# Kernel tuning notes

Measured on AMD Instinct MI355X. Metric: run time of the kernel, lower is better.

The kernel has to match this reference:

```python
import jax, jax.numpy as jnp
import numpy as np

C = 128   # channel_num
S = 56    # spatial size
K = 3     # ksize -> gaussian kernel is 2K x 2K = 6x6


def _gaussian_bank(theta, p, sig, a):
    # Vectorized version of get_gaussian over all (i, u) channel pairs.
    coords = jnp.linspace(-K, K, 2 * K)
    xv, yv = jnp.meshgrid(coords, coords, indexing='ij')  # [2K, 2K]
    ct = jnp.cos(theta)[:, :, None, None]                  # [C, C, 1, 1]
    st = jnp.sin(theta)[:, :, None, None]
    xrot = xv * ct + yv * st                               # [C, C, 2K, 2K]
    yrot = -xv * st + yv * ct
    p2 = (p ** 2)[:, :, None, None]
    s2 = (sig ** 2)[:, :, None, None]
    amp = (a / (2.0 * jnp.pi * p * sig))[:, :, None, None]
    return amp * jnp.exp(-0.5 * (xrot ** 2 / p2 + yrot ** 2 / s2))  # [C, C, 2K, 2K]


def setup_inputs() -> dict:
    key = jax.random.key(0)
    ks = jax.random.split(key, 8)
    scale = 90.0
    theta = scale * jnp.abs(jax.random.normal(ks[0], (C, C)))
    p = scale * jnp.abs(jax.random.normal(ks[1], (C, C))) + 10.0
    sig = scale * jnp.abs(jax.random.normal(ks[2], (C, C))) + 10.0
    a = scale * jnp.abs(jax.random.normal(ks[3], (C, C)))
    nI = jnp.abs(jax.random.normal(ks[4], (C, C)))
    nU = jnp.abs(jax.random.normal(ks[5], (C,)))
    bias = jnp.abs(jax.random.normal(ks[6], (C,)))
    # positive activations (module assumes post-ReLU input; pow of negatives -> NaN)
    x = jax.random.uniform(ks[7], (2, C, S, S), dtype=jnp.float32)
    return {"x": x, "theta": theta, "p": p, "sig": sig, "a": a,
            "nI": nI, "nU": nU, "bias": bias}


def reference(x, theta, p, sig, a, nI, nU, bias):
    B = x.shape[0]
    g = _gaussian_bank(theta, p, sig, a)                     # [C, C, 2K, 2K]
    # x[b,i]^nI[i,u] for all pairs -> [B, C, C, S, S]
    xp = x[:, :, None, :, :] ** nI[None, :, :, None, None]
    xp = xp.reshape(B, C * C, S, S)
    kern = g.reshape(C * C, 1, 2 * K, 2 * K)
    # depthwise cross-correlation per (i,u) pair; even kernel + pad K -> S+1,
    # then crop first row/col (matches output[1:, 1:] in the torch code)
    conv = jax.lax.conv_general_dilated(
        xp, kern, window_strides=(1, 1), padding=((K, K), (K, K)),
        feature_group_count=C * C)                           # [B, C*C, S+1, S+1]
    conv = conv[:, :, 1:, 1:].reshape(B, C, C, S, S)
    denom = (bias ** nU)[None, :, None, None] + conv.sum(axis=2)  # [B, C, S, S]
    num = x ** nU[None, :, None, None]
    return num / denom
```

## Files before the change

kernel.cpp:

```cpp
#include <hip/hip_runtime.h>
#include <math.h>

#define CN 128
#define SN 56
#define PCOLS 33
#define NPX 627
#define MT 40
#define PXPAD 654
#define GTS 136
#define DYS (6 * PXPAD + PCOLS)
#define DXS (PXPAD + 1)

typedef float  fr4 __attribute__((ext_vector_type(4)));
typedef short  sh8 __attribute__((ext_vector_type(8)));

__device__ __forceinline__ unsigned short f2bf(float f) {
    unsigned u = __float_as_uint(f);
    u += 0x7FFFu + ((u >> 16) & 1u);
    return (unsigned short)(u >> 16);
}
__device__ __forceinline__ int pk2(float f0, float f1) {
    unsigned u0 = __float_as_uint(f0) + 0x8000u;
    unsigned u1 = __float_as_uint(f1) + 0x8000u;
    return (int)__builtin_amdgcn_perm(u1, u0, 0x07060302u);
}
__device__ __forceinline__ float bf2f(unsigned short s) {
    return __uint_as_float(((unsigned)s) << 16);
}

__global__ __launch_bounds__(256, 3) void divnorm_mfma(
        const float* __restrict__ x, const float* __restrict__ theta,
        const float* __restrict__ pP, const float* __restrict__ sig,
        const float* __restrict__ aA, const float* __restrict__ nI,
        const float* __restrict__ nU, const float* __restrict__ bias,
        float* __restrict__ out)
{
    __shared__ alignas(16) unsigned short SH[36 * PXPAD];
    unsigned short* Gt = SH;

    const int bid = blockIdx.x;
    const int w   = bid & 1;
    const int h   = (bid >> 1) & 1;
    const int c   = (bid >> 2) & 127;
    const int b   = bid >> 9;
    const int tid = threadIdx.x;
    const int lane = tid & 63;
    const int wv   = tid >> 6;
    const int l15  = lane & 15;
    const int lg   = lane >> 4;

    for (int i = tid; i < 12 * GTS; i += 256) Gt[36 * GTS + i] = 0;

    for (int idx = tid; idx < CN * 36; idx += 256) {
        int u  = idx / 36;
        int tap = idx - u * 36;
        int ky = tap / 6;
        int kx = tap - ky * 6;
        int pr = c * CN + u;
        float th = theta[pr], pv = pP[pr], sv = sig[pr], av = aA[pr];
        float ct = __cosf(th), st = __sinf(th);
        float xv = -3.0f + 1.2f * ky;
        float yv = -3.0f + 1.2f * kx;
        float xr =  xv * ct + yv * st;
        float yr = -xv * st + yv * ct;
        float e  = -0.5f * (xr * xr / (pv * pv) + yr * yr / (sv * sv));
        float g  = (av / (2.0f * 3.14159265358979323846f * pv * sv))
                   * __builtin_amdgcn_exp2f(e * 1.44269504088896341f);
        Gt[tap * GTS + u] = f2bf(g);
    }

    float nIr[4][8];
    {
        const float* nc = nI + c * CN;
        #pragma unroll
        for (int ks = 0; ks < 4; ++ks) {
            const float4* q = (const float4*)(nc + ks * 32 + lg * 8);
            float4 q0 = q[0], q1 = q[1];
            nIr[ks][0] = q0.x; nIr[ks][1] = q0.y; nIr[ks][2] = q0.z; nIr[ks][3] = q0.w;
            nIr[ks][4] = q1.x; nIr[ks][5] = q1.y; nIr[ks][6] = q1.z; nIr[ks][7] = q1.w;
        }
    }

    const float* xc = x   + (size_t)(b * CN + c) * (SN * SN);
    float*       oc = out + (size_t)(b * CN + c) * (SN * SN);
    const float nUc = nU[c];
    const float bn  = __builtin_amdgcn_exp2f(nUc * __builtin_amdgcn_logf(bias[c]));
    const int   c0  = 28 * w;

    __syncthreads();

    sh8 Bf[3][4];
    #pragma unroll
    for (int nt = 0; nt < 3; ++nt)
        #pragma unroll
        for (int ks = 0; ks < 4; ++ks)
            Bf[nt][ks] = *(const sh8*)&Gt[(nt * 16 + l15) * GTS + ks * 32 + lg * 8];
    __syncthreads();

    #pragma unroll 1
    for (int band = 0; band < 2; ++band) {
        const int r0 = 28 * h + 14 * band;

        #pragma unroll 1
        for (int mt = wv; mt < MT; mt += 4) {
            int pidx = mt * 16 + l15;
            int prl  = pidx / PCOLS;
            int pcl  = pidx - prl * PCOLS;
            int prow = r0 - 2 + prl;
            int pcol = c0 - 2 + pcl;
            bool vld = ((unsigned)prow < 56u) && ((unsigned)pcol < 56u);
            float xv = xc[vld ? (prow * SN + pcol) : 0];
            float L  = vld ? __builtin_amdgcn_logf(xv) : -1e30f;

            fr4 a0 = {0.f,0.f,0.f,0.f}, a1 = {0.f,0.f,0.f,0.f}, a2 = {0.f,0.f,0.f,0.f};
            #pragma unroll
            for (int ks = 0; ks < 4; ++ks) {
                float t[8];
                #pragma unroll
                for (int j = 0; j < 8; ++j)
                    t[j] = __builtin_amdgcn_exp2f(nIr[ks][j] * L);
                int4 ai;
                ai.x = pk2(t[0], t[1]); ai.y = pk2(t[2], t[3]);
                ai.z = pk2(t[4], t[5]); ai.w = pk2(t[6], t[7]);
                sh8 af = *(sh8*)&ai;
                a0 = __builtin_amdgcn_mfma_f32_16x16x32_bf16(af, Bf[0][ks], a0, 0, 0, 0);
                a1 = __builtin_amdgcn_mfma_f32_16x16x32_bf16(af, Bf[1][ks], a1, 0, 0, 0);
                a2 = __builtin_amdgcn_mfma_f32_16x16x32_bf16(af, Bf[2][ks], a2, 0, 0, 0);
            }

            const int pbase = mt * 16 + lg * 4;
            #pragma unroll
            for (int nt = 0; nt < 3; ++nt) {
                int tap = nt * 16 + l15;
                if (tap < 36) {
                    fr4 av4 = (nt == 0) ? a0 : ((nt == 1) ? a1 : a2);
                    int* dst = (int*)&SH[tap * PXPAD + pbase];
                    dst[0] = pk2(av4[0], av4[1]);
                    dst[1] = pk2(av4[2], av4[3]);
                }
            }
        }
        __syncthreads();

        #pragma unroll
        for (int k = 0; k < 2; ++k) {
            int pp = tid + 256 * k;
            if (pp < 14 * 28) {
                int oy = pp / 28;
                int ox = pp - oy * 28;
                const unsigned short* pb = &SH[oy * PCOLS + ox];
                float s = 0.0f;
                #pragma unroll
                for (int dy = 0; dy < 6; ++dy)
                    #pragma unroll
                    for (int dx = 0; dx < 6; ++dx)
                        s += bf2f(pb[dy * DYS + dx * DXS]);
                int y  = r0 + oy;
                int xg = c0 + ox;
                float xv  = xc[y * SN + xg];
                float num = __builtin_amdgcn_exp2f(nUc * __builtin_amdgcn_logf(xv));
                oc[y * SN + xg] = num / (bn + s);
            }
        }
        __syncthreads();
    }
}

extern "C" void kernel_launch(void* const* d_in, const int* in_sizes, int n_in,
                              void* d_out, int out_size, void* d_ws, size_t ws_size,
                              hipStream_t stream) {
    const float* x     = (const float*)d_in[0];
    const float* theta = (const float*)d_in[1];
    const float* p     = (const float*)d_in[2];
    const float* sig   = (const float*)d_in[3];
    const float* a     = (const float*)d_in[4];
    const float* nI    = (const float*)d_in[5];
    const float* nU    = (const float*)d_in[6];
    const float* bias  = (const float*)d_in[7];
    float* out = (float*)d_out;

    hipLaunchKernelGGL(divnorm_mfma, dim3(2 * CN * 4), dim3(256), 0, stream,
                       x, theta, p, sig, a, nI, nU, bias, out);
}
```

Before: 120.4 us.

## Precompute Gaussian bank in MFMA fragment layout via separate kernel; use 512-thread blocks

After: 107.5 us. 10.8% less time.

```diff
diff --git a/kernel.cpp b/kernel.cpp
--- a/kernel.cpp
+++ b/kernel.cpp
@@ -4,12 +4,11 @@
 #define CN 128
 #define SN 56
 #define PCOLS 33
-#define NPX 627
-#define MT 40
 #define PXPAD 654
-#define GTS 136
+#define PXPAD_DW 327
 #define DYS (6 * PXPAD + PCOLS)
 #define DXS (PXPAD + 1)
+#define LOG2E 1.44269504088896341f
 
 typedef float  fr4 __attribute__((ext_vector_type(4)));
 typedef short  sh8 __attribute__((ext_vector_type(8)));
@@ -28,15 +27,46 @@
     return __uint_as_float(((unsigned)s) << 16);
 }
 
-__global__ __launch_bounds__(256, 3) void divnorm_mfma(
-        const float* __restrict__ x, const float* __restrict__ theta,
-        const float* __restrict__ pP, const float* __restrict__ sig,
-        const float* __restrict__ aA, const float* __restrict__ nI,
-        const float* __restrict__ nU, const float* __restrict__ bias,
-        float* __restrict__ out)
+__global__ void bank_kernel(const float* __restrict__ theta,
+                            const float* __restrict__ p,
+                            const float* __restrict__ sig,
+                            const float* __restrict__ a,
+                            unsigned short* __restrict__ bank) {
+    int t = blockIdx.x * 256 + threadIdx.x;
+    int lane = t & 63;
+    int grp  = t >> 6;
+    int nt = grp % 3;
+    int ks = (grp / 3) & 3;
+    int c  = grp / 12;
+    int tap = nt * 16 + (lane & 15);
+    int ub  = ks * 32 + (lane >> 4) * 8;
+    sh8 v = {0,0,0,0,0,0,0,0};
+    if (tap < 36) {
+        int ky = tap / 6, kx = tap - ky * 6;
+        float xv = -3.0f + 1.2f * ky;
+        float yv = -3.0f + 1.2f * kx;
+        #pragma unroll
+        for (int j = 0; j < 8; ++j) {
+            int pr = c * CN + ub + j;
+            float th = theta[pr], pv = p[pr], sv = sig[pr], av = a[pr];
+            float ct = __cosf(th), st = __sinf(th);
+            float xr =  xv * ct + yv * st;
+            float yr = -xv * st + yv * ct;
+            float e  = -0.5f * (xr * xr / (pv * pv) + yr * yr / (sv * sv));
+            float g  = (av / (2.0f * 3.14159265358979323846f * pv * sv))
+                       * __builtin_amdgcn_exp2f(e * LOG2E);
+            v[j] = (short)f2bf(g);
+        }
+    }
+    ((sh8*)bank)[t] = v;
+}
+
+__global__ __launch_bounds__(512, 4) void divnorm_mfma(
+        const float* __restrict__ x, const unsigned short* __restrict__ bank,
+        const float* __restrict__ nI, const float* __restrict__ nU,
+        const float* __restrict__ bias, float* __restrict__ out)
 {
     __shared__ alignas(16) unsigned short SH[36 * PXPAD];
-    unsigned short* Gt = SH;
 
     const int bid = blockIdx.x;
     const int w   = bid & 1;
@@ -49,24 +79,14 @@
     const int l15  = lane & 15;
     const int lg   = lane >> 4;
 
-    for (int i = tid; i < 12 * GTS; i += 256) Gt[36 * GTS + i] = 0;
-
-    for (int idx = tid; idx < CN * 36; idx += 256) {
-        int u  = idx / 36;
-        int tap = idx - u * 36;
-        int ky = tap / 6;
-        int kx = tap - ky * 6;
-        int pr = c * CN + u;
-        float th = theta[pr], pv = pP[pr], sv = sig[pr], av = aA[pr];
-        float ct = __cosf(th), st = __sinf(th);
-        float xv = -3.0f + 1.2f * ky;
-        float yv = -3.0f + 1.2f * kx;
-        float xr =  xv * ct + yv * st;
-        float yr = -xv * st + yv * ct;
-        float e  = -0.5f * (xr * xr / (pv * pv) + yr * yr / (sv * sv));
-        float g  = (av / (2.0f * 3.14159265358979323846f * pv * sv))
-                   * __builtin_amdgcn_exp2f(e * 1.44269504088896341f);
-        Gt[tap * GTS + u] = f2bf(g);
+    sh8 Bf[3][4];
+    {
+        const sh8* bp = (const sh8*)bank + (size_t)c * 768 + lane;
+        #pragma unroll
+        for (int ks = 0; ks < 4; ++ks)
+            #pragma unroll
+            for (int nt = 0; nt < 3; ++nt)
+                Bf[nt][ks] = bp[(ks * 3 + nt) * 64];
     }
 
     float nIr[4][8];
@@ -85,32 +105,39 @@
     float*       oc = out + (size_t)(b * CN + c) * (SN * SN);
     const float nUc = nU[c];
     const float bn  = __builtin_amdgcn_exp2f(nUc * __builtin_amdgcn_logf(bias[c]));
-    const int   c0  = 28 * w;
-
-    __syncthreads();
-
-    sh8 Bf[3][4];
-    #pragma unroll
-    for (int nt = 0; nt < 3; ++nt)
-        #pragma unroll
-        for (int ks = 0; ks < 4; ++ks)
-            Bf[nt][ks] = *(const sh8*)&Gt[(nt * 16 + l15) * GTS + ks * 32 + lg * 8];
-    __syncthreads();
+    const int   c0m2 = 28 * w - 2;
+
+    const int pof0 = l15 * PXPAD_DW;
+    const int pof1 = (16 + l15) * PXPAD_DW;
+    const int pof2 = (32 + l15) * PXPAD_DW;
 
     #pragma unroll 1
     for (int band = 0; band < 2; ++band) {
-        const int r0 = 28 * h + 14 * band;
+        const int r0   = 28 * h + 14 * band;
+        const int r0m2 = r0 - 2;
+
+        int pidx = wv * 16 + l15;
+        int prl  = pidx / PCOLS;
+        int pcl  = pidx - prl * PCOLS;
+        int prow = r0m2 + prl;
+        int pcol = c0m2 + pcl;
+        bool val = ((unsigned)prow < 56u) && ((unsigned)pcol < 56u);
+        float xv = xc[val ? (prow * SN + pcol) : 0];
 
         #pragma unroll 1
-        for (int mt = wv; mt < MT; mt += 4) {
-            int pidx = mt * 16 + l15;
-            int prl  = pidx / PCOLS;
-            int pcl  = pidx - prl * PCOLS;
-            int prow = r0 - 2 + prl;
-            int pcol = c0 - 2 + pcl;
-            bool vld = ((unsigned)prow < 56u) && ((unsigned)pcol < 56u);
-            float xv = xc[vld ? (prow * SN + pcol) : 0];
-            float L  = vld ? __builtin_amdgcn_logf(xv) : -1e30f;
+        for (int i = 0; i < 5; ++i) {
+            float L = val ? __builtin_amdgcn_logf(xv) : -1e30f;
+
+            {
+                int np   = pidx + 128;
+                int nprl = np / PCOLS;
+                int npcl = np - nprl * PCOLS;
+                int nprw = r0m2 + nprl;
+                int npcc = c0m2 + npcl;
+                val = ((unsigned)nprw < 56u) && ((unsigned)npcc < 56u);
+                xv  = xc[val ? (nprw * SN + npcc) : 0];
+                pidx = np;
+            }
 
             fr4 a0 = {0.f,0.f,0.f,0.f}, a1 = {0.f,0.f,0.f,0.f}, a2 = {0.f,0.f,0.f,0.f};
             #pragma unroll
@@ -128,39 +155,34 @@
                 a2 = __builtin_amdgcn_mfma_f32_16x16x32_bf16(af, Bf[2][ks], a2, 0, 0, 0);
             }
 
-            const int pbase = mt * 16 + lg * 4;
+            int pbd = (wv + 8 * i) * 8 + lg * 2;
+            int* SD = (int*)SH;
+            SD[pof0 + pbd]     = pk2(a0[0], a0[1]);
+            SD[pof0 + pbd + 1] = pk2(a0[2], a0[3]);
+            SD[pof1 + pbd]     = pk2(a1[0], a1[1]);
+            SD[pof1 + pbd + 1] = pk2(a1[2], a1[3]);
+            if (l15 < 4) {
+                SD[pof2 + pbd]     = pk2(a2[0], a2[1]);
+                SD[pof2 + pbd + 1] = pk2(a2[2], a2[3]);
+            }
+        }
+        __syncthreads();
+
+        if (tid < 14 * 28) {
+            int oy = tid / 28;
+            int ox = tid - oy * 28;
+            const unsigned short* pb = &SH[oy * PCOLS + ox];
+            float s = 0.0f;
             #pragma unroll
-            for (int nt = 0; nt < 3; ++nt) {
-                int tap = nt * 16 + l15;
-                if (tap < 36) {
-                    fr4 av4 = (nt == 0) ? a0 : ((nt == 1) ? a1 : a2);
-                    int* dst = (int*)&SH[tap * PXPAD + pbase];
-                    dst[0] = pk2(av4[0], av4[1]);
-                    dst[1] = pk2(av4[2], av4[3]);
-                }
-            }
-        }
-        __syncthreads();
-
-        #pragma unroll
-        for (int k = 0; k < 2; ++k) {
-            int pp = tid + 256 * k;
-            if (pp < 14 * 28) {
-                int oy = pp / 28;
-                int ox = pp - oy * 28;
-                const unsigned short* pb = &SH[oy * PCOLS + ox];
-                float s = 0.0f;
+            for (int dy = 0; dy < 6; ++dy)
                 #pragma unroll
-                for (int dy = 0; dy < 6; ++dy)
-                    #pragma unroll
-                    for (int dx = 0; dx < 6; ++dx)
-                        s += bf2f(pb[dy * DYS + dx * DXS]);
-                int y  = r0 + oy;
-                int xg = c0 + ox;
-                float xv  = xc[y * SN + xg];
-                float num = __builtin_amdgcn_exp2f(nUc * __builtin_amdgcn_logf(xv));
-                oc[y * SN + xg] = num / (bn + s);
-            }
+                for (int dx = 0; dx < 6; ++dx)
+                    s += bf2f(pb[dy * DYS + dx * DXS]);
+            int y  = r0 + oy;
+            int xg = c0m2 + 2 + ox;
+            float xq  = xc[y * SN + xg];
+            float num = __builtin_amdgcn_exp2f(nUc * __builtin_amdgcn_logf(xq));
+            oc[y * SN + xg] = num / (bn + s);
         }
         __syncthreads();
     }
@@ -178,7 +200,10 @@
     const float* nU    = (const float*)d_in[6];
     const float* bias  = (const float*)d_in[7];
     float* out = (float*)d_out;
-
-    hipLaunchKernelGGL(divnorm_mfma, dim3(2 * CN * 4), dim3(256), 0, stream,
-                       x, theta, p, sig, a, nI, nU, bias, out);
-}
+    unsigned short* bank = (unsigned short*)d_ws;
+
+    hipLaunchKernelGGL(bank_kernel, dim3(384), dim3(256), 0, stream,
+                       theta, p, sig, a, bank);
+    hipLaunchKernelGGL(divnorm_mfma, dim3(2 * CN * 4), dim3(512), 0, stream,
+                       x, bank, nI, nU, bias, out);
+}
```
